# Optimization experiments

Hardware: AMD Instinct MI355X
Metric: run time of the kernel (lower is better)

## Reference

```python
import jax, jax.numpy as jnp
import numpy as np

N_USERS = 100000
N_ITEMS = 50000
N_NODES = N_USERS + N_ITEMS
N_INTER = 3200000
DIM = 64
N_LAYERS = 3


def setup_inputs() -> dict:
    key = jax.random.key(0)
    k1, k2, k3, k4, k5, k6 = jax.random.split(key, 6)
    # Embedding tables, init N(0, 0.1) as in nn.init.normal_(std=0.1)
    user_emb = 0.1 * jax.random.normal(k1, (N_USERS, DIM), dtype=jnp.float32)
    item_emb = 0.1 * jax.random.normal(k2, (N_ITEMS, DIM), dtype=jnp.float32)
    # Random bipartite interactions, symmetrized
    u = jax.random.randint(k3, (N_INTER,), 0, N_USERS, dtype=jnp.int32)
    i = jax.random.randint(k4, (N_INTER,), 0, N_ITEMS, dtype=jnp.int32) + N_USERS
    edge_src = jnp.concatenate([u, i])  # [2*N_INTER]
    edge_dst = jnp.concatenate([i, u])
    # Symmetric normalization D^-1/2 A D^-1/2 (as in getSparseGraph)
    deg = jax.ops.segment_sum(jnp.ones_like(edge_src, dtype=jnp.float32), edge_src,
                              num_segments=N_NODES)
    d_inv_sqrt = jnp.where(deg > 0, 1.0 / jnp.sqrt(deg), 0.0)
    edge_val = d_inv_sqrt[edge_src] * d_inv_sqrt[edge_dst]
    users = jax.random.randint(k5, (4096,), 0, N_USERS, dtype=jnp.int32)
    items = jax.random.randint(k6, (4096,), 0, N_ITEMS, dtype=jnp.int32)
    return {"user_emb": user_emb, "item_emb": item_emb,
            "edge_src": edge_src, "edge_dst": edge_dst, "edge_val": edge_val,
            "users": users, "items": items}


def _spmm(edge_src, edge_dst, edge_val, x):
    # y[r] = sum_{e: src[e]=r} val[e] * x[dst[e]]
    return jax.ops.segment_sum(edge_val[:, None] * x[edge_dst], edge_src,
                               num_segments=N_NODES)


def reference(user_emb, item_emb, edge_src, edge_dst, edge_val, users, items):
    all_emb = jnp.concatenate([user_emb, item_emb], axis=0)  # [N_NODES, D]
    acc = all_emb
    emb = all_emb
    for _ in range(N_LAYERS):
        emb = _spmm(edge_src, edge_dst, edge_val, emb)
        acc = acc + emb
    light_out = acc / jnp.asarray(N_LAYERS + 1, dtype=all_emb.dtype)
    all_users = light_out[:N_USERS]
    all_items = light_out[N_USERS:]
    u = all_users[users]  # [B, D]
    v = all_items[items]  # [B, D]
    gamma = jnp.sum(u * v, axis=1)  # [B]
    return gamma
```

## Files before the change

### kernel.cpp

```cpp
#include <hip/hip_runtime.h>

#define N_USERS 100000
#define N_ITEMS 50000
#define N_NODES 150000
#define DIM 64
#define NQ 4096
#define GROUP 1024
#define NG ((N_NODES + GROUP - 1) / GROUP)
#define NBLK_A 512
#define NT (NG * NBLK_A)
#define NSB2 ((NT + 1023) / 1024)

typedef __attribute__((ext_vector_type(4))) _Float16 h4;
typedef __attribute__((ext_vector_type(8))) _Float16 h8;

static inline size_t align256(size_t x) { return (x + 255) & ~(size_t)255; }

__global__ void k_concat_w(const float* __restrict__ ue, const float* __restrict__ ie,
                           const float* __restrict__ dis, h4* __restrict__ w) {
    int i = blockIdx.x * blockDim.x + threadIdx.x;
    const int totalU = N_USERS * 16;
    const int total  = N_NODES * 16;
    if (i >= total) return;
    float4 v = (i < totalU) ? ((const float4*)ue)[i] : ((const float4*)ie)[i - totalU];
    float s = dis[i >> 4];
    h4 o;
    o.x = (_Float16)(v.x * s); o.y = (_Float16)(v.y * s);
    o.z = (_Float16)(v.z * s); o.w = (_Float16)(v.w * s);
    w[i] = o;
}

__global__ void k_count(const int* __restrict__ src, int* __restrict__ T,
                        int nE, int epb) {
    __shared__ int h[NG];
    int tid = threadIdx.x, b = blockIdx.x;
    for (int i = tid; i < NG; i += 256) h[i] = 0;
    __syncthreads();
    int e0 = b * epb, e1 = min(e0 + epb, nE);
    for (int rb = e0; rb < e1; rb += 1024) {
        int e = rb + tid * 4;
        if (e + 3 < e1) {
            int4 s4 = *(const int4*)(src + e);
            atomicAdd(&h[s4.x >> 10], 1);
            atomicAdd(&h[s4.y >> 10], 1);
            atomicAdd(&h[s4.z >> 10], 1);
            atomicAdd(&h[s4.w >> 10], 1);
        } else {
            for (int j = 0; j < 4; ++j) {
                int ee = e + j;
                if (ee < e1) atomicAdd(&h[src[ee] >> 10], 1);
            }
        }
    }
    __syncthreads();
    for (int i = tid; i < NG; i += 256) T[i * NBLK_A + b] = h[i];
}

__global__ void k_scan1(int* __restrict__ T, int* __restrict__ btot) {
    __shared__ int ws[4];
    int blk = blockIdx.x, tid = threadIdx.x;
    int lane = tid & 63, wid = tid >> 6;
    int idx = blk * 1024 + tid * 4;
    int a0 = 0, a1 = 0, a2 = 0, a3 = 0;
    if (idx + 3 < NT) {
        int4 v = *(const int4*)(T + idx);
        a0 = v.x; a1 = v.y; a2 = v.z; a3 = v.w;
    } else {
        if (idx     < NT) a0 = T[idx];
        if (idx + 1 < NT) a1 = T[idx + 1];
        if (idx + 2 < NT) a2 = T[idx + 2];
        if (idx + 3 < NT) a3 = T[idx + 3];
    }
    int s = a0 + a1 + a2 + a3;
    int x = s;
#pragma unroll
    for (int off = 1; off < 64; off <<= 1) {
        int t = __shfl_up(x, off);
        if (lane >= off) x += t;
    }
    if (lane == 63) ws[wid] = x;
    __syncthreads();
    int woff = 0;
    for (int w = 0; w < wid; ++w) woff += ws[w];
    int excl = woff + x - s;
    if (idx + 3 < NT) {
        int4 o; o.x = excl; o.y = excl + a0; o.z = excl + a0 + a1; o.w = excl + a0 + a1 + a2;
        *(int4*)(T + idx) = o;
    } else {
        if (idx     < NT) T[idx]     = excl;
        if (idx + 1 < NT) T[idx + 1] = excl + a0;
        if (idx + 2 < NT) T[idx + 2] = excl + a0 + a1;
        if (idx + 3 < NT) T[idx + 3] = excl + a0 + a1 + a2;
    }
    if (tid == 255) btot[blk] = woff + x;
}

__global__ void k_scan2(int* __restrict__ btot) {
    __shared__ int ws[4];
    int tid = threadIdx.x, lane = tid & 63, wid = tid >> 6;
    int v = (tid < NSB2) ? btot[tid] : 0;
    int x = v;
#pragma unroll
    for (int off = 1; off < 64; off <<= 1) {
        int t = __shfl_up(x, off);
        if (lane >= off) x += t;
    }
    if (lane == 63) ws[wid] = x;
    __syncthreads();
    int woff = 0;
    for (int w = 0; w < wid; ++w) woff += ws[w];
    if (tid < NSB2) btot[tid] = woff + x - v;
}

__global__ void k_scan3(int* __restrict__ T, const int* __restrict__ btot) {
    int blk = blockIdx.x, tid = threadIdx.x;
    int idx = blk * 1024 + tid * 4;
    int add = btot[blk];
    if (idx + 3 < NT) {
        int4 v = *(int4*)(T + idx);
        v.x += add; v.y += add; v.z += add; v.w += add;
        *(int4*)(T + idx) = v;
    } else {
        if (idx     < NT) T[idx]     += add;
        if (idx + 1 < NT) T[idx + 1] += add;
        if (idx + 2 < NT) T[idx + 2] += add;
    }
}

__global__ void k_scatterb(const int* __restrict__ src, const int* __restrict__ dst,
                           const int* __restrict__ T, unsigned int* __restrict__ brec,
                           int nE, int epb) {
    __shared__ int base_[NG];
    __shared__ int cur[NG];
    int tid = threadIdx.x, b = blockIdx.x;
    for (int i = tid; i < NG; i += 256) { base_[i] = T[i * NBLK_A + b]; cur[i] = 0; }
    __syncthreads();
    int e0 = b * epb, e1 = min(e0 + epb, nE);
    for (int rb = e0; rb < e1; rb += 1024) {
        int e = rb + tid * 4;
        if (e + 3 < e1) {
            int4 s4 = *(const int4*)(src + e);
            int4 d4 = *(const int4*)(dst + e);
#pragma unroll
            for (int j = 0; j < 4; ++j) {
                int s = (j == 0) ? s4.x : (j == 1) ? s4.y : (j == 2) ? s4.z : s4.w;
                int d = (j == 0) ? d4.x : (j == 1) ? d4.y : (j == 2) ? d4.z : d4.w;
                int g = s >> 10;
                int c = atomicAdd(&cur[g], 1);
                brec[base_[g] + c] = ((unsigned int)(s & 1023) << 18) | (unsigned int)d;
            }
        } else {
            for (int j = 0; j < 4; ++j) {
                int ee = e + j;
                if (ee < e1) {
                    int s = src[ee];
                    int d = dst[ee];
                    int g = s >> 10;
                    int c = atomicAdd(&cur[g], 1);
                    brec[base_[g] + c] = ((unsigned int)(s & 1023) << 18) | (unsigned int)d;
                }
            }
        }
    }
}

__global__ void k_place(const int* __restrict__ T, const unsigned int* __restrict__ brec,
                        int* __restrict__ rowp, float* __restrict__ dis,
                        float* __restrict__ dis2, float* __restrict__ rdis,
                        int* __restrict__ cdst, int nE) {
    __shared__ int cnt[GROUP];
    __shared__ int ws[16];
    int g   = blockIdx.x;
    int nlo = g * GROUP;
    int gn  = min(GROUP, N_NODES - nlo);
    int tid = threadIdx.x;
    int lane = tid & 63, wid = tid >> 6;
    cnt[tid] = 0;
    __syncthreads();
    int beg  = T[g * NBLK_A];
    int endr = (g == NG - 1) ? nE : T[(g + 1) * NBLK_A];
    for (int i = beg + tid; i < endr; i += blockDim.x)
        atomicAdd(&cnt[brec[i] >> 18], 1);
    __syncthreads();
    int mycnt = cnt[tid];
    int x = mycnt;
#pragma unroll
    for (int off = 1; off < 64; off <<= 1) {
        int t = __shfl_up(x, off);
        if (lane >= off) x += t;
    }
    if (lane == 63) ws[wid] = x;
    __syncthreads();
    if (wid == 0 && lane < 16) {
        int s = ws[lane];
        int y = s;
#pragma unroll
        for (int off = 1; off < 16; off <<= 1) {
            int t = __shfl_up(y, off);
            if (lane >= off) y += t;
        }
        ws[lane] = y - s;
    }
    __syncthreads();
    int excl = ws[wid] + x - mycnt;
    if (tid < gn) {
        rowp[nlo + tid] = beg + excl;
        float c = (float)mycnt;
        dis [nlo + tid] = (mycnt > 0) ? 1.0f / sqrtf(c) : 0.0f;
        dis2[nlo + tid] = (mycnt > 0) ? 1.0f / c        : 0.0f;
        rdis[nlo + tid] = (mycnt > 0) ? sqrtf(c)        : 0.0f;
    }
    if (g == NG - 1 && tid == 0) rowp[N_NODES] = nE;
    cnt[tid] = beg + excl;
    __syncthreads();
    for (int i = beg + tid; i < endr; i += blockDim.x) {
        unsigned int rec = brec[i];
        int s = (int)(rec >> 18);
        int d = (int)(rec & 0x3FFFFu);
        int pos = atomicAdd(&cnt[s], 1);
        cdst[pos] = d;
    }
}

__global__ void k_spmm_w(const int* __restrict__ rowp, const int* __restrict__ cdst,
                         const float* __restrict__ dis2, const h8* __restrict__ x8,
                         h8* __restrict__ y8) {
    int gw   = (blockIdx.x * blockDim.x + threadIdx.x) >> 6;
    int lane = threadIdx.x & 63;
    if (gw >= N_NODES) return;
    int beg = rowp[gw], end = rowp[gw + 1];
    int g8 = lane >> 3;
    int k  = lane & 7;
    float acc[8] = {0.f, 0.f, 0.f, 0.f, 0.f, 0.f, 0.f, 0.f};
    int len = end - beg;
    int n32 = len & ~31;
    int p = beg;
    for (; p < beg + n32; p += 32) {
        int e0 = p + g8, e1 = e0 + 8, e2 = e0 + 16, e3 = e0 + 24;
        int d0 = cdst[e0], d1 = cdst[e1], d2 = cdst[e2], d3 = cdst[e3];
        h8 a = x8[(size_t)d0 * 8 + k];
        h8 b = x8[(size_t)d1 * 8 + k];
        h8 c = x8[(size_t)d2 * 8 + k];
        h8 d = x8[(size_t)d3 * 8 + k];
#pragma unroll
        for (int j = 0; j < 8; ++j)
            acc[j] += ((float)a[j] + (float)b[j]) + ((float)c[j] + (float)d[j]);
    }
    for (; p + g8 < end; p += 8) {
        int d = cdst[p + g8];
        h8 a = x8[(size_t)d * 8 + k];
#pragma unroll
        for (int j = 0; j < 8; ++j)
            acc[j] += (float)a[j];
    }
#pragma unroll
    for (int off = 8; off < 64; off <<= 1) {
#pragma unroll
        for (int j = 0; j < 8; ++j)
            acc[j] += __shfl_xor(acc[j], off);
    }
    if (lane < 8) {
        float s = dis2[gw];
        h8 o;
#pragma unroll
        for (int j = 0; j < 8; ++j) o[j] = (_Float16)(acc[j] * s);
        y8[(size_t)gw * 8 + lane] = o;
    }
}

__global__ void k_spmm_q(const int* __restrict__ users, const int* __restrict__ items,
                         const int* __restrict__ rowp, const int* __restrict__ cdst,
                         const float* __restrict__ dis, const h8* __restrict__ x8,
                         float* __restrict__ acc) {
    int r    = (blockIdx.x * blockDim.x + threadIdx.x) >> 6;
    int lane = threadIdx.x & 63;
    if (r >= 2 * NQ) return;
    int node = (r < NQ) ? users[r] : (N_USERS + items[r - NQ]);
    int beg = rowp[node], end = rowp[node + 1];
    int g8 = lane >> 3;
    int k  = lane & 7;
    float s[8] = {0.f, 0.f, 0.f, 0.f, 0.f, 0.f, 0.f, 0.f};
    int len = end - beg;
    int n32 = len & ~31;
    int p = beg;
    for (; p < beg + n32; p += 32) {
        int e0 = p + g8, e1 = e0 + 8, e2 = e0 + 16, e3 = e0 + 24;
        int d0 = cdst[e0], d1 = cdst[e1], d2 = cdst[e2], d3 = cdst[e3];
        h8 a = x8[(size_t)d0 * 8 + k];
        h8 b = x8[(size_t)d1 * 8 + k];
        h8 c = x8[(size_t)d2 * 8 + k];
        h8 d = x8[(size_t)d3 * 8 + k];
#pragma unroll
        for (int j = 0; j < 8; ++j)
            s[j] += ((float)a[j] + (float)b[j]) + ((float)c[j] + (float)d[j]);
    }
    for (; p + g8 < end; p += 8) {
        int d = cdst[p + g8];
        h8 a = x8[(size_t)d * 8 + k];
#pragma unroll
        for (int j = 0; j < 8; ++j)
            s[j] += (float)a[j];
    }
#pragma unroll
    for (int off = 8; off < 64; off <<= 1) {
#pragma unroll
        for (int j = 0; j < 8; ++j)
            s[j] += __shfl_xor(s[j], off);
    }
    if (lane < 8) {
        float dr = dis[node];
        float* ap = acc + (size_t)r * DIM + lane * 8;
        float4 c0 = *(float4*)ap;
        float4 c1 = *(float4*)(ap + 4);
        c0.x += s[0] * dr; c0.y += s[1] * dr; c0.z += s[2] * dr; c0.w += s[3] * dr;
        c1.x += s[4] * dr; c1.y += s[5] * dr; c1.z += s[6] * dr; c1.w += s[7] * dr;
        *(float4*)ap = c0;
        *(float4*)(ap + 4) = c1;
    }
}

__global__ void k_gather_init(const int* __restrict__ users, const int* __restrict__ items,
                              const float* __restrict__ ue, const float* __restrict__ ie,
                              float* __restrict__ acc) {
    int t = blockIdx.x * blockDim.x + threadIdx.x;
    int r = t >> 4;
    int k = t & 15;
    if (r >= 2 * NQ) return;
    float4 v;
    if (r < NQ) v = ((const float4*)ue)[(size_t)users[r] * 16 + k];
    else        v = ((const float4*)ie)[(size_t)items[r - NQ] * 16 + k];
    ((float4*)acc)[(size_t)r * 16 + k] = v;
}

__global__ void k_gather_w(const int* __restrict__ users, const int* __restrict__ items,
                           const float* __restrict__ rdis, const h4* __restrict__ w,
                           float* __restrict__ acc) {
    int t = blockIdx.x * blockDim.x + threadIdx.x;
    int r = t >> 4;
    int k = t & 15;
    if (r >= 2 * NQ) return;
    int node = (r < NQ) ? users[r] : (N_USERS + items[r - NQ]);
    h4 v = w[(size_t)node * 16 + k];
    float s = rdis[node];
    float4* a = ((float4*)acc) + (size_t)r * 16 + k;
    float4 c = *a;
    c.x += s * (float)v.x; c.y += s * (float)v.y;
    c.z += s * (float)v.z; c.w += s * (float)v.w;
    *a = c;
}

__global__ void k_dot(const float* __restrict__ acc, float* __restrict__ out) {
    int i = blockIdx.x * blockDim.x + threadIdx.x;
    if (i >= NQ) return;
    const float* u = acc + (size_t)i * DIM;
    const float* v = acc + (size_t)(NQ + i) * DIM;
    float s = 0.f;
#pragma unroll
    for (int d = 0; d < DIM; ++d) s += u[d] * v[d];
    out[i] = s * (1.0f / 16.0f);
}

__global__ void k_spmm_atomic(const int* __restrict__ src, const int* __restrict__ dst,
                              const float* __restrict__ val, const float* __restrict__ x,
                              float* __restrict__ y, int nE) {
    int t = blockIdx.x * blockDim.x + threadIdx.x;
    int e = t >> 4;
    int k = t & 15;
    if (e >= nE) return;
    int   s = src[e];
    int   d = dst[e];
    float v = val[e];
    float4 xv = ((const float4*)x)[(size_t)d * 16 + k];
    float* yp = y + (size_t)s * DIM + k * 4;
    atomicAdd(yp + 0, v * xv.x);
    atomicAdd(yp + 1, v * xv.y);
    atomicAdd(yp + 2, v * xv.z);
    atomicAdd(yp + 3, v * xv.w);
}

__global__ void k_concat(const float* __restrict__ ue, const float* __restrict__ ie,
                         float* __restrict__ emb) {
    int i = blockIdx.x * blockDim.x + threadIdx.x;
    const int totalU = N_USERS * DIM / 4;
    const int total  = N_NODES * DIM / 4;
    if (i >= total) return;
    float4 v = (i < totalU) ? ((const float4*)ue)[i] : ((const float4*)ie)[i - totalU];
    ((float4*)emb)[i] = v;
}

__global__ void k_gather(const int* __restrict__ users, const int* __restrict__ items,
                         const float* __restrict__ emb, float* __restrict__ acc,
                         int init) {
    int t = blockIdx.x * blockDim.x + threadIdx.x;
    int r = t >> 4;
    int k = t & 15;
    if (r >= 2 * NQ) return;
    int node = (r < NQ) ? users[r] : (N_USERS + items[r - NQ]);
    float4 v = ((const float4*)emb)[(size_t)node * 16 + k];
    float4* a = ((float4*)acc) + (size_t)r * 16 + k;
    if (init) {
        *a = v;
    } else {
        float4 c = *a;
        c.x += v.x; c.y += v.y; c.z += v.z; c.w += v.w;
        *a = c;
    }
}

extern "C" void kernel_launch(void* const* d_in, const int* in_sizes, int n_in,
                              void* d_out, int out_size, void* d_ws, size_t ws_size,
                              hipStream_t stream) {
    const float* ue    = (const float*)d_in[0];
    const float* ie    = (const float*)d_in[1];
    const int*   esrc  = (const int*)d_in[2];
    const int*   edst  = (const int*)d_in[3];
    const float* ev    = (const float*)d_in[4];
    const int*   users = (const int*)d_in[5];
    const int*   items = (const int*)d_in[6];
    float* out = (float*)d_out;
    const int nE = in_sizes[2];

    const size_t embHB = (size_t)N_NODES * DIM * sizeof(_Float16);
    const size_t accB  = (size_t)2 * NQ * DIM * sizeof(float);
    const size_t rpB   = (size_t)(N_NODES + 1) * sizeof(int);
    const size_t disB  = (size_t)N_NODES * sizeof(float);
    const size_t tB    = (size_t)NT * sizeof(int);
    const size_t btB   = (size_t)NSB2 * sizeof(int);
    const size_t cdB   = (size_t)nE * sizeof(int);

    size_t o = 0;
    char* base = (char*)d_ws;
    h4*    w0    = (h4*)   (base + o); o = align256(o + embHB);
    h4*    w1    = (h4*)   (base + o); o = align256(o + embHB);
    float* acc   = (float*)(base + o); o = align256(o + accB);
    int*   rowp  = (int*)  (base + o); o = align256(o + rpB);
    float* dis   = (float*)(base + o); o = align256(o + disB);
    float* dis2  = (float*)(base + o); o = align256(o + disB);
    float* rdis  = (float*)(base + o); o = align256(o + disB);
    int*   T     = (int*)  (base + o); o = align256(o + tB);
    int*   btot  = (int*)  (base + o); o = align256(o + btB);
    int*   cdst  = (int*)  (base + o); o = align256(o + cdB);
    unsigned int* brec = (unsigned int*)(base + o); o = align256(o + cdB);
    const bool csr_ok = (o <= ws_size);

    if (csr_ok) {
        int epb = ((nE + NBLK_A - 1) / NBLK_A + 3) & ~3;

        k_count<<<NBLK_A, 256, 0, stream>>>(esrc, T, nE, epb);
        k_scan1<<<NSB2, 256, 0, stream>>>(T, btot);
        k_scan2<<<1, 256, 0, stream>>>(btot);
        k_scan3<<<NSB2, 256, 0, stream>>>(T, btot);
        k_scatterb<<<NBLK_A, 256, 0, stream>>>(esrc, edst, T, brec, nE, epb);
        k_place<<<NG, 1024, 0, stream>>>(T, brec, rowp, dis, dis2, rdis, cdst, nE);

        const int totalH4 = N_NODES * 16;
        k_concat_w<<<(totalH4 + 255) / 256, 256, 0, stream>>>(ue, ie, dis, w0);
        k_gather_init<<<(2 * NQ * 16 + 255) / 256, 256, 0, stream>>>(users, items, ue, ie, acc);

        h4* cur = w0;
        h4* nxt = w1;
        const int spmmBlocks = (N_NODES * 64 + 255) / 256;
        for (int l = 0; l < 2; ++l) {
            k_spmm_w<<<spmmBlocks, 256, 0, stream>>>(rowp, cdst, dis2, (const h8*)cur, (h8*)nxt);
            k_gather_w<<<(2 * NQ * 16 + 255) / 256, 256, 0, stream>>>(users, items, rdis, nxt, acc);
            h4* tmp = cur; cur = nxt; nxt = tmp;
        }
        k_spmm_q<<<(2 * NQ * 64 + 255) / 256, 256, 0, stream>>>(users, items, rowp, cdst, dis,
                                                                (const h8*)cur, acc);
    } else {
        const size_t embB = (size_t)N_NODES * DIM * sizeof(float);
        size_t o2 = 0;
        float* emb0 = (float*)(base + o2); o2 = align256(o2 + embB);
        float* emb1 = (float*)(base + o2); o2 = align256(o2 + embB);
        float* acc2 = (float*)(base + o2); o2 = align256(o2 + accB);
        acc = acc2;
        const int totalV4 = N_NODES * DIM / 4;
        k_concat<<<(totalV4 + 255) / 256, 256, 0, stream>>>(ue, ie, emb0);
        k_gather<<<(2 * NQ * 16 + 255) / 256, 256, 0, stream>>>(users, items, emb0, acc, 1);
        float* cur = emb0;
        float* nxt = emb1;
        for (int l = 0; l < 3; ++l) {
            hipMemsetAsync(nxt, 0, embB, stream);
            long threads = (long)nE * 16;
            k_spmm_atomic<<<(int)((threads + 255) / 256), 256, 0, stream>>>(esrc, edst, ev, cur, nxt, nE);
            k_gather<<<(2 * NQ * 16 + 255) / 256, 256, 0, stream>>>(users, items, nxt, acc, 0);
            float* tmp = cur; cur = nxt; nxt = tmp;
        }
    }

    k_dot<<<(NQ + 255) / 256, 256, 0, stream>>>(acc, out);
}
```

Baseline: 351.7 us.

## Fuse embedding scaling into placement and merge query gather, last layer and dot

The separate concat/scale kernel is folded into the tail of k_place, which now reads user/item embeddings and writes the scaled fp16 layer-0 buffer using the per-block degree values in shared memory. The init gather and first gather are merged into one kernel that combines the raw embedding with the layer-1 result. The last-layer query SpMM, the final gather and the dot product are fused into a single k_tail kernel with one block per query pair. This cuts several small launches and round trips of the accumulator through memory, at the cost of a longer k_place and less parallelism inside each tail block.

```diff
diff --git a/kernel.cpp b/kernel.cpp
--- a/kernel.cpp
+++ b/kernel.cpp
@@ -15,20 +15,6 @@
 typedef __attribute__((ext_vector_type(8))) _Float16 h8;
 
 static inline size_t align256(size_t x) { return (x + 255) & ~(size_t)255; }
-
-__global__ void k_concat_w(const float* __restrict__ ue, const float* __restrict__ ie,
-                           const float* __restrict__ dis, h4* __restrict__ w) {
-    int i = blockIdx.x * blockDim.x + threadIdx.x;
-    const int totalU = N_USERS * 16;
-    const int total  = N_NODES * 16;
-    if (i >= total) return;
-    float4 v = (i < totalU) ? ((const float4*)ue)[i] : ((const float4*)ie)[i - totalU];
-    float s = dis[i >> 4];
-    h4 o;
-    o.x = (_Float16)(v.x * s); o.y = (_Float16)(v.y * s);
-    o.z = (_Float16)(v.z * s); o.w = (_Float16)(v.w * s);
-    w[i] = o;
-}
 
 __global__ void k_count(const int* __restrict__ src, int* __restrict__ T,
                         int nE, int epb) {
@@ -165,10 +151,12 @@
 }
 
 __global__ void k_place(const int* __restrict__ T, const unsigned int* __restrict__ brec,
+                        const float* __restrict__ ue, const float* __restrict__ ie,
                         int* __restrict__ rowp, float* __restrict__ dis,
                         float* __restrict__ dis2, float* __restrict__ rdis,
-                        int* __restrict__ cdst, int nE) {
+                        int* __restrict__ cdst, h4* __restrict__ w0, int nE) {
     __shared__ int cnt[GROUP];
+    __shared__ float sdis[GROUP];
     __shared__ int ws[16];
     int g   = blockIdx.x;
     int nlo = g * GROUP;
@@ -203,12 +191,15 @@
     }
     __syncthreads();
     int excl = ws[wid] + x - mycnt;
+    float dv = 0.0f;
+    if (mycnt > 0) dv = 1.0f / sqrtf((float)mycnt);
+    sdis[tid] = dv;
     if (tid < gn) {
         rowp[nlo + tid] = beg + excl;
         float c = (float)mycnt;
-        dis [nlo + tid] = (mycnt > 0) ? 1.0f / sqrtf(c) : 0.0f;
-        dis2[nlo + tid] = (mycnt > 0) ? 1.0f / c        : 0.0f;
-        rdis[nlo + tid] = (mycnt > 0) ? sqrtf(c)        : 0.0f;
+        dis [nlo + tid] = dv;
+        dis2[nlo + tid] = (mycnt > 0) ? 1.0f / c : 0.0f;
+        rdis[nlo + tid] = (mycnt > 0) ? sqrtf(c) : 0.0f;
     }
     if (g == NG - 1 && tid == 0) rowp[N_NODES] = nE;
     cnt[tid] = beg + excl;
@@ -219,6 +210,21 @@
         int d = (int)(rec & 0x3FFFFu);
         int pos = atomicAdd(&cnt[s], 1);
         cdst[pos] = d;
+    }
+    for (int r0 = 0; r0 < gn; r0 += 64) {
+        int rl = r0 + (tid >> 4);
+        if (rl < gn) {
+            int node = nlo + rl;
+            int kk = tid & 15;
+            float4 v = (node < N_USERS)
+                ? ((const float4*)ue)[(size_t)node * 16 + kk]
+                : ((const float4*)ie)[(size_t)(node - N_USERS) * 16 + kk];
+            float s = sdis[rl];
+            h4 o;
+            o.x = (_Float16)(v.x * s); o.y = (_Float16)(v.y * s);
+            o.z = (_Float16)(v.z * s); o.w = (_Float16)(v.w * s);
+            w0[(size_t)node * 16 + kk] = o;
+        }
     }
 }
 
@@ -268,14 +274,37 @@
     }
 }
 
-__global__ void k_spmm_q(const int* __restrict__ users, const int* __restrict__ items,
-                         const int* __restrict__ rowp, const int* __restrict__ cdst,
-                         const float* __restrict__ dis, const h8* __restrict__ x8,
-                         float* __restrict__ acc) {
-    int r    = (blockIdx.x * blockDim.x + threadIdx.x) >> 6;
-    int lane = threadIdx.x & 63;
+__global__ void k_gather_w1(const int* __restrict__ users, const int* __restrict__ items,
+                            const float* __restrict__ ue, const float* __restrict__ ie,
+                            const float* __restrict__ rdis, const h4* __restrict__ w1,
+                            float* __restrict__ acc) {
+    int t = blockIdx.x * blockDim.x + threadIdx.x;
+    int r = t >> 4;
+    int k = t & 15;
     if (r >= 2 * NQ) return;
     int node = (r < NQ) ? users[r] : (N_USERS + items[r - NQ]);
+    float4 v = (node < N_USERS)
+        ? ((const float4*)ue)[(size_t)node * 16 + k]
+        : ((const float4*)ie)[(size_t)(node - N_USERS) * 16 + k];
+    h4 wv = w1[(size_t)node * 16 + k];
+    float s = rdis[node];
+    float4 c;
+    c.x = v.x + s * (float)wv.x; c.y = v.y + s * (float)wv.y;
+    c.z = v.z + s * (float)wv.z; c.w = v.w + s * (float)wv.w;
+    ((float4*)acc)[(size_t)r * 16 + k] = c;
+}
+
+__global__ void k_tail(const int* __restrict__ users, const int* __restrict__ items,
+                       const int* __restrict__ rowp, const int* __restrict__ cdst,
+                       const float* __restrict__ dis, const float* __restrict__ rdis,
+                       const h8* __restrict__ x8, const float* __restrict__ acc,
+                       float* __restrict__ out) {
+    __shared__ float buf[2][64];
+    int b = blockIdx.x;
+    int w = threadIdx.x >> 6;
+    int lane = threadIdx.x & 63;
+    int r = b + w * NQ;
+    int node = (w == 0) ? users[b] : (N_USERS + items[b]);
     int beg = rowp[node], end = rowp[node + 1];
     int g8 = lane >> 3;
     int k  = lane & 7;
@@ -287,12 +316,12 @@
         int e0 = p + g8, e1 = e0 + 8, e2 = e0 + 16, e3 = e0 + 24;
         int d0 = cdst[e0], d1 = cdst[e1], d2 = cdst[e2], d3 = cdst[e3];
         h8 a = x8[(size_t)d0 * 8 + k];
-        h8 b = x8[(size_t)d1 * 8 + k];
+        h8 bb = x8[(size_t)d1 * 8 + k];
         h8 c = x8[(size_t)d2 * 8 + k];
         h8 d = x8[(size_t)d3 * 8 + k];
 #pragma unroll
         for (int j = 0; j < 8; ++j)
-            s[j] += ((float)a[j] + (float)b[j]) + ((float)c[j] + (float)d[j]);
+            s[j] += ((float)a[j] + (float)bb[j]) + ((float)c[j] + (float)d[j]);
     }
     for (; p + g8 < end; p += 8) {
         int d = cdst[p + g8];
@@ -308,56 +337,20 @@
             s[j] += __shfl_xor(s[j], off);
     }
     if (lane < 8) {
-        float dr = dis[node];
-        float* ap = acc + (size_t)r * DIM + lane * 8;
-        float4 c0 = *(float4*)ap;
-        float4 c1 = *(float4*)(ap + 4);
-        c0.x += s[0] * dr; c0.y += s[1] * dr; c0.z += s[2] * dr; c0.w += s[3] * dr;
-        c1.x += s[4] * dr; c1.y += s[5] * dr; c1.z += s[6] * dr; c1.w += s[7] * dr;
-        *(float4*)ap = c0;
-        *(float4*)(ap + 4) = c1;
-    }
-}
-
-__global__ void k_gather_init(const int* __restrict__ users, const int* __restrict__ items,
-                              const float* __restrict__ ue, const float* __restrict__ ie,
-                              float* __restrict__ acc) {
-    int t = blockIdx.x * blockDim.x + threadIdx.x;
-    int r = t >> 4;
-    int k = t & 15;
-    if (r >= 2 * NQ) return;
-    float4 v;
-    if (r < NQ) v = ((const float4*)ue)[(size_t)users[r] * 16 + k];
-    else        v = ((const float4*)ie)[(size_t)items[r - NQ] * 16 + k];
-    ((float4*)acc)[(size_t)r * 16 + k] = v;
-}
-
-__global__ void k_gather_w(const int* __restrict__ users, const int* __restrict__ items,
-                           const float* __restrict__ rdis, const h4* __restrict__ w,
-                           float* __restrict__ acc) {
-    int t = blockIdx.x * blockDim.x + threadIdx.x;
-    int r = t >> 4;
-    int k = t & 15;
-    if (r >= 2 * NQ) return;
-    int node = (r < NQ) ? users[r] : (N_USERS + items[r - NQ]);
-    h4 v = w[(size_t)node * 16 + k];
-    float s = rdis[node];
-    float4* a = ((float4*)acc) + (size_t)r * 16 + k;
-    float4 c = *a;
-    c.x += s * (float)v.x; c.y += s * (float)v.y;
-    c.z += s * (float)v.z; c.w += s * (float)v.w;
-    *a = c;
-}
-
-__global__ void k_dot(const float* __restrict__ acc, float* __restrict__ out) {
-    int i = blockIdx.x * blockDim.x + threadIdx.x;
-    if (i >= NQ) return;
-    const float* u = acc + (size_t)i * DIM;
-    const float* v = acc + (size_t)(NQ + i) * DIM;
-    float s = 0.f;
-#pragma unroll
-    for (int d = 0; d < DIM; ++d) s += u[d] * v[d];
-    out[i] = s * (1.0f / 16.0f);
+        float dn = dis[node], rn = rdis[node];
+        h8 wr = x8[(size_t)node * 8 + lane];
+        const float* ap = acc + (size_t)r * DIM + lane * 8;
+#pragma unroll
+        for (int j = 0; j < 8; ++j)
+            buf[w][lane * 8 + j] = ap[j] + rn * (float)wr[j] + dn * s[j];
+    }
+    __syncthreads();
+    if (w == 0) {
+        float pd = buf[0][lane] * buf[1][lane];
+#pragma unroll
+        for (int off = 1; off < 64; off <<= 1) pd += __shfl_xor(pd, off);
+        if (lane == 0) out[b] = pd * (1.0f / 16.0f);
+    }
 }
 
 __global__ void k_spmm_atomic(const int* __restrict__ src, const int* __restrict__ dst,
@@ -407,6 +400,17 @@
     }
 }
 
+__global__ void k_dot(const float* __restrict__ acc, float* __restrict__ out) {
+    int i = blockIdx.x * blockDim.x + threadIdx.x;
+    if (i >= NQ) return;
+    const float* u = acc + (size_t)i * DIM;
+    const float* v = acc + (size_t)(NQ + i) * DIM;
+    float s = 0.f;
+#pragma unroll
+    for (int d = 0; d < DIM; ++d) s += u[d] * v[d];
+    out[i] = s * (1.0f / 16.0f);
+}
+
 extern "C" void kernel_launch(void* const* d_in, const int* in_sizes, int n_in,
                               void* d_out, int out_size, void* d_ws, size_t ws_size,
                               hipStream_t stream) {
@@ -451,42 +455,34 @@
         k_scan2<<<1, 256, 0, stream>>>(btot);
         k_scan3<<<NSB2, 256, 0, stream>>>(T, btot);
         k_scatterb<<<NBLK_A, 256, 0, stream>>>(esrc, edst, T, brec, nE, epb);
-        k_place<<<NG, 1024, 0, stream>>>(T, brec, rowp, dis, dis2, rdis, cdst, nE);
-
-        const int totalH4 = N_NODES * 16;
-        k_concat_w<<<(totalH4 + 255) / 256, 256, 0, stream>>>(ue, ie, dis, w0);
-        k_gather_init<<<(2 * NQ * 16 + 255) / 256, 256, 0, stream>>>(users, items, ue, ie, acc);
-
-        h4* cur = w0;
-        h4* nxt = w1;
+        k_place<<<NG, 1024, 0, stream>>>(T, brec, ue, ie, rowp, dis, dis2, rdis,
+                                         cdst, w0, nE);
+
         const int spmmBlocks = (N_NODES * 64 + 255) / 256;
-        for (int l = 0; l < 2; ++l) {
-            k_spmm_w<<<spmmBlocks, 256, 0, stream>>>(rowp, cdst, dis2, (const h8*)cur, (h8*)nxt);
-            k_gather_w<<<(2 * NQ * 16 + 255) / 256, 256, 0, stream>>>(users, items, rdis, nxt, acc);
-            h4* tmp = cur; cur = nxt; nxt = tmp;
-        }
-        k_spmm_q<<<(2 * NQ * 64 + 255) / 256, 256, 0, stream>>>(users, items, rowp, cdst, dis,
-                                                                (const h8*)cur, acc);
+        k_spmm_w<<<spmmBlocks, 256, 0, stream>>>(rowp, cdst, dis2, (const h8*)w0, (h8*)w1);
+        k_gather_w1<<<(2 * NQ * 16 + 255) / 256, 256, 0, stream>>>(users, items, ue, ie,
+                                                                   rdis, w1, acc);
+        k_spmm_w<<<spmmBlocks, 256, 0, stream>>>(rowp, cdst, dis2, (const h8*)w1, (h8*)w0);
+        k_tail<<<NQ, 128, 0, stream>>>(users, items, rowp, cdst, dis, rdis,
+                                       (const h8*)w0, acc, out);
     } else {
         const size_t embB = (size_t)N_NODES * DIM * sizeof(float);
         size_t o2 = 0;
         float* emb0 = (float*)(base + o2); o2 = align256(o2 + embB);
         float* emb1 = (float*)(base + o2); o2 = align256(o2 + embB);
         float* acc2 = (float*)(base + o2); o2 = align256(o2 + accB);
-        acc = acc2;
         const int totalV4 = N_NODES * DIM / 4;
         k_concat<<<(totalV4 + 255) / 256, 256, 0, stream>>>(ue, ie, emb0);
-        k_gather<<<(2 * NQ * 16 + 255) / 256, 256, 0, stream>>>(users, items, emb0, acc, 1);
+        k_gather<<<(2 * NQ * 16 + 255) / 256, 256, 0, stream>>>(users, items, emb0, acc2, 1);
         float* cur = emb0;
         float* nxt = emb1;
         for (int l = 0; l < 3; ++l) {
             hipMemsetAsync(nxt, 0, embB, stream);
             long threads = (long)nE * 16;
             k_spmm_atomic<<<(int)((threads + 255) / 256), 256, 0, stream>>>(esrc, edst, ev, cur, nxt, nE);
-            k_gather<<<(2 * NQ * 16 + 255) / 256, 256, 0, stream>>>(users, items, nxt, acc, 0);
+            k_gather<<<(2 * NQ * 16 + 255) / 256, 256, 0, stream>>>(users, items, nxt, acc2, 0);
             float* tmp = cur; cur = nxt; nxt = tmp;
         }
-    }
-
-    k_dot<<<(NQ + 255) / 256, 256, 0, stream>>>(acc, out);
-}
+        k_dot<<<(NQ + 255) / 256, 256, 0, stream>>>(acc2, out);
+    }
+}
```

Result: faster. 339.2 us (-3.5%).
